# Performance work log

Measured on AMD Instinct MI355X. Metric: run time of the kernel, lower is better.

## Reference

```python
import jax, jax.numpy as jnp
import numpy as np
import math

D_MODEL = 1024
NUM_HEADS = 16
HEAD_DIM = D_MODEL // NUM_HEADS
BLOCK_SIZE = 64
THRESHOLD = 0.99


def setup_inputs() -> dict:
    key = jax.random.key(0)
    ks = jax.random.split(key, 12)
    B, S, D = 2, 2048, D_MODEL
    scale = 1.0 / math.sqrt(D)
    x = jax.random.normal(ks[0], (B, S, D), dtype=jnp.float32)
    G_ii = jax.random.uniform(ks[1], (B, S), dtype=jnp.float32)
    # Linear weights stored as [in, out]; applied as x @ W + b (matches nn.Linear math).
    Wq = jax.random.normal(ks[2], (D, D), dtype=jnp.float32) * scale
    bq = jnp.zeros((D,), dtype=jnp.float32)
    Wk = jax.random.normal(ks[3], (D, D), dtype=jnp.float32) * scale
    bk = jnp.zeros((D,), dtype=jnp.float32)
    Wv = jax.random.normal(ks[4], (D, D), dtype=jnp.float32) * scale
    bv = jnp.zeros((D,), dtype=jnp.float32)
    Wo = jax.random.normal(ks[5], (D, D), dtype=jnp.float32) * scale
    bo = jnp.zeros((D,), dtype=jnp.float32)
    return {"x": x, "G_ii": G_ii, "Wq": Wq, "bq": bq, "Wk": Wk, "bk": bk,
            "Wv": Wv, "bv": bv, "Wo": Wo, "bo": bo}


def reference(x, G_ii, Wq, bq, Wk, bk, Wv, bv, Wo, bo):
    B, S, D = x.shape
    H, hd, bs = NUM_HEADS, HEAD_DIM, BLOCK_SIZE
    nb = S // bs

    # Projections and head split: [B, H, S, hd]
    q = (x @ Wq + bq).reshape(B, S, H, hd).transpose(0, 2, 1, 3)
    k = (x @ Wk + bk).reshape(B, S, H, hd).transpose(0, 2, 1, 3)
    v = (x @ Wv + bv).reshape(B, S, H, hd).transpose(0, 2, 1, 3)

    # Per-query-block scattering energy keep mask: block kept iff max |G_ii| >= threshold
    energy = jnp.abs(G_ii)                              # [B, S]
    block_max = energy.reshape(B, nb, bs).max(axis=-1)  # [B, nb]
    keep = (block_max >= THRESHOLD)                     # [B, nb] bool
    row_keep = jnp.repeat(keep, bs, axis=1)             # [B, S]

    # Kept query blocks attend densely (non-causal) over all keys; skipped blocks output zero.
    scores = jnp.einsum('bhqd,bhkd->bhqk', q, k) / math.sqrt(hd)  # [B, H, S, S]
    attn = jax.nn.softmax(scores, axis=-1)
    out = jnp.einsum('bhqk,bhkd->bhqd', attn, v)                  # [B, H, S, hd]
    out = out * row_keep[:, None, :, None].astype(out.dtype)

    out = out.transpose(0, 2, 1, 3).reshape(B, S, D)
    return out @ Wo + bo
```

## Files before the change

### kernel.cpp

```cpp
#include <hip/hip_runtime.h>
#include <math.h>

#define D_MODEL   1024
#define NUM_HEADS 16
#define HEAD_DIM  64
#define BS        64
#define NB        32
#define S_LEN     2048
#define BATCH     2
#define M_ROWS    (BATCH * S_LEN)
#define THRESH    0.99f
#define SCEXP     0.18033688f
#define SPLITK    4
#define NSLOT     66
#define SLOTB     (NSLOT * 16)

typedef __attribute__((ext_vector_type(8))) short bf16x8;
typedef __attribute__((ext_vector_type(8))) _Float16 f16x8;
typedef __attribute__((ext_vector_type(2))) __fp16 fp16v2;
typedef __attribute__((ext_vector_type(4))) float f32x4;

__device__ __forceinline__ unsigned short f2bf(float f) {
    unsigned int u = __float_as_uint(f);
    u += 0x7fff + ((u >> 16) & 1);
    return (unsigned short)(u >> 16);
}

__device__ __forceinline__ unsigned int pkrtz(float a, float b) {
    fp16v2 r = __builtin_amdgcn_cvt_pkrtz(a, b);
    return __builtin_bit_cast(unsigned int, r);
}

__device__ __forceinline__ void gload16(const void* gptr, void* lptr) {
    __builtin_amdgcn_global_load_lds(
        (const __attribute__((address_space(1))) void*)gptr,
        (__attribute__((address_space(3))) void*)lptr, 16, 0, 0);
}

__global__ __launch_bounds__(256) void prep_kernel(
    const float* __restrict__ x, const float* __restrict__ G,
    const float* __restrict__ Wq, const float* __restrict__ Wk,
    const float* __restrict__ Wv, const float* __restrict__ Wo,
    unsigned short* __restrict__ xb, unsigned short* __restrict__ wcat,
    unsigned short* __restrict__ wot, int* __restrict__ keep, int* __restrict__ work)
{
    const int bid = blockIdx.x, tid = threadIdx.x;
    __shared__ float T[64][65];

    if (bid < 2048) {
        size_t i = ((size_t)bid * 256 + tid) * 8;
        float4 a = *(const float4*)(x + i);
        float4 b = *(const float4*)(x + i + 4);
        uint4 o;
        o.x = (unsigned int)f2bf(a.x) | ((unsigned int)f2bf(a.y) << 16);
        o.y = (unsigned int)f2bf(a.z) | ((unsigned int)f2bf(a.w) << 16);
        o.z = (unsigned int)f2bf(b.x) | ((unsigned int)f2bf(b.y) << 16);
        o.w = (unsigned int)f2bf(b.z) | ((unsigned int)f2bf(b.w) << 16);
        *(uint4*)(xb + i) = o;
    } else if (bid < 3072) {
        int i = bid - 2048;
        int mat = i >> 8, rem = i & 255;
        int k0 = (rem & 15) * 64, n0 = (rem >> 4) * 64;
        const float* W = (mat == 0) ? Wq : (mat == 1) ? Wk : (mat == 2) ? Wv : Wo;
        int rr = tid >> 4, c4 = (tid & 15) * 4;
        #pragma unroll
        for (int j = 0; j < 4; j++) {
            int row = rr + j * 16;
            float4 v = *(const float4*)(W + (size_t)(k0 + row) * 1024 + n0 + c4);
            T[row][c4 + 0] = v.x; T[row][c4 + 1] = v.y;
            T[row][c4 + 2] = v.z; T[row][c4 + 3] = v.w;
        }
        __syncthreads();
        unsigned short* dst = (mat < 3) ? (wcat + (size_t)mat * 1024 * 1024) : wot;
        #pragma unroll
        for (int j = 0; j < 4; j++) {
            int n = rr + j * 16;
            unsigned int lo = (unsigned int)f2bf(T[c4 + 0][n]) | ((unsigned int)f2bf(T[c4 + 1][n]) << 16);
            unsigned int hi = (unsigned int)f2bf(T[c4 + 2][n]) | ((unsigned int)f2bf(T[c4 + 3][n]) << 16);
            *(uint2*)(dst + (size_t)(n0 + n) * 1024 + k0 + c4) = make_uint2(lo, hi);
        }
    } else {
        if (tid < 64) {
            int t = tid;
            const float4* g = (const float4*)(G + (size_t)t * 64);
            float mx = 0.f;
            #pragma unroll
            for (int j = 0; j < 16; j++) {
                float4 v = g[j];
                mx = fmaxf(mx, fmaxf(fmaxf(fabsf(v.x), fabsf(v.y)), fmaxf(fabsf(v.z), fabsf(v.w))));
            }
            bool k = (mx >= THRESH);
            unsigned long long bal = __ballot(k);
            unsigned int mk0 = (unsigned int)bal, mk1 = (unsigned int)(bal >> 32);
            int nk0 = __popc(mk0), nk1 = __popc(mk1);
            int ND0 = (nk0 + 1) >> 1, ND1 = (nk1 + 1) >> 1;
            keep[t] = k ? 1 : 0;
            int tb = t & 31, bb = t >> 5;
            unsigned int mb = bb ? mk1 : mk0;
            unsigned int msk = (tb == 0) ? 0u : ((1u << tb) - 1u);
            int rank = __popc(mb & msk);
            int rd   = __popc(~mb & msk);
            int base = bb ? 2 * ND0 : 0;
            int dbase = 2 * ND0 + 2 * ND1;
            int doff = bb ? (32 - nk0) : 0;
            if (k)  work[1 + base + rank] = t;
            else    work[1 + dbase + doff + rd] = t | (1 << 8);
            if (t == 0) {
                work[0] = ND0 + ND1;
                if (nk0 & 1) work[1 + nk0] = (31 - __clz(mk0)) | (2 << 8);
                if (nk1 & 1) work[1 + 2 * ND0 + nk1] = (63 - __clz(mk1)) | (2 << 8);
                int total = dbase + (64 - nk0 - nk1);
                for (int j = total; j < NSLOT; j++) work[1 + j] = (2 << 8);
            }
        }
    }
}

__global__ __launch_bounds__(256, 3) void gemm_qkv(
    const unsigned short* __restrict__ A, const unsigned short* __restrict__ Bt,
    const float* __restrict__ bq, const float* __restrict__ bk, const float* __restrict__ bv,
    const int* __restrict__ keep, unsigned short* __restrict__ qk, unsigned short* __restrict__ vt)
{
    const int n0 = blockIdx.x * 128, m0 = blockIdx.y * 128;
    const int tid = threadIdx.x, w = tid >> 6, lane = tid & 63;
    const int quad = lane >> 4, l16 = lane & 15;
    const int wm = w >> 1, wn = w & 1;
    const int kindb = n0 >> 10;
    if (kindb == 0 && !(keep[2 * blockIdx.y] | keep[2 * blockIdx.y + 1])) return;

    __shared__ union {
        struct { unsigned short As[2][128 * 32]; unsigned short Bs[2][128 * 32]; } s;
        unsigned short qkr[128 * 136];
        unsigned short vr[128 * 136];
    } u;

    f32x4 acc[4][4];
    #pragma unroll
    for (int mt = 0; mt < 4; mt++)
        #pragma unroll
        for (int nt = 0; nt < 4; nt++) acc[mt][nt] = (f32x4){0.f, 0.f, 0.f, 0.f};

    #define QSTAGE(it_, p_)                                                             \
        {                                                                               \
            int k0_ = (it_) * 32;                                                       \
            _Pragma("unroll")                                                           \
            for (int j = 0; j < 2; j++) {                                               \
                int s_ = w * 128 + j * 64 + lane; int row = s_ >> 2, cl = s_ & 3;       \
                int c = cl ^ ((row >> 1) & 3);                                          \
                gload16(A + (size_t)(m0 + row) * 1024 + k0_ + c * 8,                    \
                        &u.s.As[p_][(w * 128 + j * 64) * 8]);                           \
            }                                                                           \
            _Pragma("unroll")                                                           \
            for (int j = 0; j < 2; j++) {                                               \
                int s_ = w * 128 + j * 64 + lane; int row = s_ >> 2, cl = s_ & 3;       \
                int c = cl ^ ((row >> 1) & 3);                                          \
                gload16(Bt + (size_t)(n0 + row) * 1024 + k0_ + c * 8,                   \
                        &u.s.Bs[p_][(w * 128 + j * 64) * 8]);                           \
            }                                                                           \
        }

    QSTAGE(0, 0)

    for (int it = 0; it < 32; it++) {
        const int p = it & 1;
        __syncthreads();
        if (it + 1 < 32) QSTAGE(it + 1, (it + 1) & 1)

        bf16x8 af[4], bfr[4];
        #pragma unroll
        for (int mt = 0; mt < 4; mt++) {
            int row = wm * 64 + mt * 16 + l16;
            int cl = quad ^ ((row >> 1) & 3);
            af[mt] = *(const bf16x8*)&u.s.As[p][(row * 4 + cl) * 8];
        }
        #pragma unroll
        for (int nt = 0; nt < 4; nt++) {
            int row = wn * 64 + nt * 16 + l16;
            int cl = quad ^ ((row >> 1) & 3);
            bfr[nt] = *(const bf16x8*)&u.s.Bs[p][(row * 4 + cl) * 8];
        }
        #pragma unroll
        for (int mt = 0; mt < 4; mt++)
            #pragma unroll
            for (int nt = 0; nt < 4; nt++)
                acc[mt][nt] = __builtin_amdgcn_mfma_f32_16x16x32_bf16(af[mt], bfr[nt], acc[mt][nt], 0, 0, 0);
    }
    __syncthreads();

    if (kindb < 2) {
        const float* bp = (kindb == 0) ? bq : bk;
        const float sc = (kindb == 0) ? SCEXP : 1.0f;
        #pragma unroll
        for (int nt = 0; nt < 4; nt++) {
            int coll = wn * 64 + nt * 16 + l16;
            float bb = bp[(n0 & 1023) + coll];
            #pragma unroll
            for (int mt = 0; mt < 4; mt++)
                #pragma unroll
                for (int r = 0; r < 4; r++) {
                    int row = wm * 64 + mt * 16 + quad * 4 + r;
                    u.qkr[row * 136 + coll] = f2bf((acc[mt][nt][r] + bb) * sc);
                }
        }
        __syncthreads();
        #pragma unroll
        for (int i = 0; i < 8; i++) {
            int s_ = tid + i * 256;
            int row = s_ >> 4, c16 = s_ & 15;
            uint4 v = *(const uint4*)&u.qkr[row * 136 + c16 * 8];
            *(uint4*)(qk + (size_t)(m0 + row) * 2048 + n0 + c16 * 8) = v;
        }
    } else {
        #pragma unroll
        for (int nt = 0; nt < 4; nt++) {
            int coll = wn * 64 + nt * 16 + l16;
            float bb = bv[(n0 - 2048) + coll];
            #pragma unroll
            for (int mt = 0; mt < 4; mt++) {
                int s0 = wm * 64 + mt * 16 + quad * 4;
                uint2 pv;
                pv.x = pkrtz(acc[mt][nt][0] + bb, acc[mt][nt][1] + bb);
                pv.y = pkrtz(acc[mt][nt][2] + bb, acc[mt][nt][3] + bb);
                *(uint2*)&u.vr[coll * 136 + s0] = pv;
            }
        }
        __syncthreads();
        const int b_ = m0 >> 11, sbase = m0 & 2047;
        #pragma unroll
        for (int i = 0; i < 8; i++) {
            int s_ = tid + i * 256;
            int coll = s_ >> 4, ch = s_ & 15;
            uint4 v = *(const uint4*)&u.vr[coll * 136 + ch * 8];
            int colg = n0 - 2048 + coll;
            int h_ = colg >> 6, d = colg & 63;
            *(uint4*)(vt + ((size_t)(b_ * NUM_HEADS + h_) * HEAD_DIM + d) * 2048 + sbase + ch * 8) = v;
        }
    }
}

__global__ __launch_bounds__(256, 4) void gemm_out(
    const unsigned short* __restrict__ A, const unsigned short* __restrict__ Bt,
    const float* __restrict__ bo, const int* __restrict__ keep, float* __restrict__ out)
{
    const int n0 = blockIdx.x * 64, m0 = blockIdx.y * 64;
    const int tid = threadIdx.x, w = tid >> 6, lane = tid & 63;
    const int quad = lane >> 4, l16 = lane & 15;
    const int wm = w >> 1, wn = w & 1;

    if (!keep[blockIdx.y]) {
        #pragma unroll
        for (int i = 0; i < 4; i++) {
            int s_ = tid + i * 256;
            int row = s_ >> 4, c = (s_ & 15) * 4;
            *(float4*)(out + (size_t)(m0 + row) * 1024 + n0 + c) = *(const float4*)(bo + n0 + c);
        }
        return;
    }

    __shared__ unsigned short Asl[2][64 * 32];
    __shared__ unsigned short Bsl[2][64 * 32];

    f32x4 acc[2][2];
    #pragma unroll
    for (int mt = 0; mt < 2; mt++)
        #pragma unroll
        for (int nt = 0; nt < 2; nt++) acc[mt][nt] = (f32x4){0.f, 0.f, 0.f, 0.f};

    #define OSTAGE(it_, p_)                                                             \
        {                                                                               \
            int k0_ = (it_) * 32;                                                       \
            int s_ = w * 64 + lane; int row = s_ >> 2, cl = s_ & 3;                     \
            int c = cl ^ ((row >> 1) & 3);                                              \
            gload16(A  + (size_t)(m0 + row) * 1024 + k0_ + c * 8, &Asl[p_][(w * 64) * 8]); \
            gload16(Bt + (size_t)(n0 + row) * 1024 + k0_ + c * 8, &Bsl[p_][(w * 64) * 8]); \
        }

    OSTAGE(0, 0)

    for (int it = 0; it < 32; it++) {
        const int p = it & 1;
        __syncthreads();
        if (it + 1 < 32) OSTAGE(it + 1, (it + 1) & 1)

        bf16x8 af[2], bfr[2];
        #pragma unroll
        for (int mt = 0; mt < 2; mt++) {
            int row = wm * 32 + mt * 16 + l16;
            int cl = quad ^ ((row >> 1) & 3);
            af[mt] = *(const bf16x8*)&Asl[p][(row * 4 + cl) * 8];
        }
        #pragma unroll
        for (int nt = 0; nt < 2; nt++) {
            int row = wn * 32 + nt * 16 + l16;
            int cl = quad ^ ((row >> 1) & 3);
            bfr[nt] = *(const bf16x8*)&Bsl[p][(row * 4 + cl) * 8];
        }
        #pragma unroll
        for (int mt = 0; mt < 2; mt++)
            #pragma unroll
            for (int nt = 0; nt < 2; nt++)
                acc[mt][nt] = __builtin_amdgcn_mfma_f32_16x16x32_bf16(af[mt], bfr[nt], acc[mt][nt], 0, 0, 0);
    }

    #pragma unroll
    for (int nt = 0; nt < 2; nt++) {
        int col = n0 + wn * 32 + nt * 16 + l16;
        float bb = bo[col];
        #pragma unroll
        for (int mt = 0; mt < 2; mt++) {
            int mb = m0 + wm * 32 + mt * 16 + quad * 4;
            #pragma unroll
            for (int r = 0; r < 4; r++)
                out[(size_t)(mb + r) * 1024 + col] = acc[mt][nt][r] + bb;
        }
    }
}

__global__ __launch_bounds__(256, 3) void attn_kernel(
    const unsigned short* __restrict__ qk, const unsigned short* __restrict__ Vtg,
    const int* __restrict__ work,
    unsigned short* __restrict__ opart, float* __restrict__ lpart)
{
    const int bx = blockIdx.x, half = blockIdx.y;
    const int dpair = bx >> 4, h = bx & 15;
    const int tid  = threadIdx.x;
    const int w    = tid >> 6, lane = tid & 63;
    const int quad = lane >> 4, l16 = lane & 15;

    if (dpair >= work[0]) return;
    const int j0 = 2 * dpair, j1 = j0 + 1;
    const int t0 = work[1 + j0] & 63, t1 = work[1 + j1] & 63;
    const int b = t0 >> 5, qb0 = t0 & 31, qb1 = t1 & 31;

    __shared__ unsigned short Kbuf[2][BS * HEAD_DIM];
    __shared__ unsigned short Vbuf[2][HEAD_DIM * BS];
    __shared__ unsigned short Pt[4][2][16 * 64];

    const int KEYS = S_LEN / SPLITK;
    const int NCH  = KEYS / BS;
    const unsigned short* Qb = qk + (size_t)(b * S_LEN) * 2048 + h * 64;
    const unsigned short* Kb = qk + (size_t)(b * S_LEN + half * KEYS) * 2048 + 1024 + h * 64;
    const unsigned short* Vb = Vtg + (size_t)(b * NUM_HEADS + h) * HEAD_DIM * 2048 + half * KEYS;

    const int qrow0 = qb0 * BS + w * 16 + l16;
    const int qrow1 = qb1 * BS + w * 16 + l16;
    bf16x8 qf0[2], qf1[2];
    #pragma unroll
    for (int ks = 0; ks < 2; ks++) {
        qf0[ks] = *(const bf16x8*)(Qb + (size_t)qrow0 * 2048 + ks * 32 + quad * 8);
        qf1[ks] = *(const bf16x8*)(Qb + (size_t)qrow1 * 2048 + ks * 32 + quad * 8);
    }

    f32x4 o0[4], o1[4];
    #pragma unroll
    for (int mt = 0; mt < 4; mt++) { o0[mt] = (f32x4){0.f,0.f,0.f,0.f}; o1[mt] = (f32x4){0.f,0.f,0.f,0.f}; }
    float l0 = 0.f, l1 = 0.f;

    const int sA = w * 128 + lane, sB = sA + 64;
    const int rA = sA >> 3, cA = (sA & 7) ^ (rA & 7);
    const int rB = sB >> 3, cB = (sB & 7) ^ (rB & 7);
    const size_t koA = (size_t)rA * 2048 + cA * 8, koB = (size_t)rB * 2048 + cB * 8;

    uint4 kr0, kr1, vr0, vr1;
    #define LOADREGS(kc_)                                                       \
        {                                                                       \
            const unsigned short* kg_ = Kb + (size_t)(kc_) * BS * 2048;         \
            const unsigned short* vg_ = Vb + (size_t)(kc_) * BS;                \
            kr0 = *(const uint4*)(kg_ + koA); kr1 = *(const uint4*)(kg_ + koB); \
            vr0 = *(const uint4*)(vg_ + koA); vr1 = *(const uint4*)(vg_ + koB); \
        }
    #define WRITELDS(pb_)                                                       \
        {                                                                       \
            *(uint4*)&Kbuf[pb_][(size_t)sA * 8] = kr0;                          \
            *(uint4*)&Kbuf[pb_][(size_t)sB * 8] = kr1;                          \
            *(uint4*)&Vbuf[pb_][(size_t)sA * 8] = vr0;                          \
            *(uint4*)&Vbuf[pb_][(size_t)sB * 8] = vr1;                          \
        }

    LOADREGS(0)
    WRITELDS(0)
    __syncthreads();

    #pragma unroll
    for (int kc = 0; kc < NCH; kc++) {
        const int p = kc & 1;
        if (kc + 1 < NCH) LOADREGS(kc + 1)

        f32x4 st0[4], st1[4];
        __builtin_amdgcn_s_setprio(1);
        #pragma unroll
        for (int mt = 0; mt < 4; mt++) {
            f32x4 a0 = {0.f,0.f,0.f,0.f}, a1 = {0.f,0.f,0.f,0.f};
            #pragma unroll
            for (int ks = 0; ks < 2; ks++) {
                int kk = mt * 16 + l16;
                bf16x8 kf = *(const bf16x8*)&Kbuf[p][(size_t)(kk * 8 + ((ks * 4 + quad) ^ (kk & 7))) * 8];
                a0 = __builtin_amdgcn_mfma_f32_16x16x32_bf16(kf, qf0[ks], a0, 0, 0, 0);
                a1 = __builtin_amdgcn_mfma_f32_16x16x32_bf16(kf, qf1[ks], a1, 0, 0, 0);
            }
            st0[mt] = a0; st1[mt] = a1;
        }
        __builtin_amdgcn_s_setprio(0);

        float sum0 = 0.f, sum1 = 0.f;
        #pragma unroll
        for (int mt = 0; mt < 4; mt++) {
            int c16 = 2 * mt + (quad >> 1);
            int off = (c16 ^ (l16 & 7)) * 8 + (quad & 1) * 4;
            float e00 = __builtin_amdgcn_exp2f(st0[mt][0]);
            float e01 = __builtin_amdgcn_exp2f(st0[mt][1]);
            float e02 = __builtin_amdgcn_exp2f(st0[mt][2]);
            float e03 = __builtin_amdgcn_exp2f(st0[mt][3]);
            sum0 += (e00 + e01) + (e02 + e03);
            *(uint2*)&Pt[w][0][l16 * 64 + off] = make_uint2(pkrtz(e00, e01), pkrtz(e02, e03));
            float e10 = __builtin_amdgcn_exp2f(st1[mt][0]);
            float e11 = __builtin_amdgcn_exp2f(st1[mt][1]);
            float e12 = __builtin_amdgcn_exp2f(st1[mt][2]);
            float e13 = __builtin_amdgcn_exp2f(st1[mt][3]);
            sum1 += (e10 + e11) + (e12 + e13);
            *(uint2*)&Pt[w][1][l16 * 64 + off] = make_uint2(pkrtz(e10, e11), pkrtz(e12, e13));
        }
        sum0 += __shfl_xor(sum0, 16, 64);
        sum0 += __shfl_xor(sum0, 32, 64);
        sum1 += __shfl_xor(sum1, 16, 64);
        sum1 += __shfl_xor(sum1, 32, 64);
        l0 += sum0; l1 += sum1;

        __builtin_amdgcn_s_setprio(1);
        #pragma unroll
        for (int ks = 0; ks < 2; ks++) {
            int poff = ((4 * ks + quad) ^ (l16 & 7)) * 8;
            f16x8 pf0 = *(const f16x8*)&Pt[w][0][l16 * 64 + poff];
            f16x8 pf1 = *(const f16x8*)&Pt[w][1][l16 * 64 + poff];
            #pragma unroll
            for (int mt = 0; mt < 4; mt++) {
                int d = mt * 16 + l16;
                f16x8 vf = *(const f16x8*)&Vbuf[p][(size_t)(d * 8 + ((ks * 4 + quad) ^ (d & 7))) * 8];
                o0[mt] = __builtin_amdgcn_mfma_f32_16x16x32_f16(vf, pf0, o0[mt], 0, 0, 0);
                o1[mt] = __builtin_amdgcn_mfma_f32_16x16x32_f16(vf, pf1, o1[mt], 0, 0, 0);
            }
        }
        __builtin_amdgcn_s_setprio(0);

        if (kc + 1 < NCH) {
            WRITELDS(p ^ 1)
            __syncthreads();
        }
    }

    {
        unsigned short* ob = opart + ((size_t)(half * SLOTB + j0 * 16 + h)) * 4096 + tid * 16;
        uint4 w0, w1;
        w0.x = pkrtz(o0[0][0], o0[0][1]); w0.y = pkrtz(o0[0][2], o0[0][3]);
        w0.z = pkrtz(o0[1][0], o0[1][1]); w0.w = pkrtz(o0[1][2], o0[1][3]);
        w1.x = pkrtz(o0[2][0], o0[2][1]); w1.y = pkrtz(o0[2][2], o0[2][3]);
        w1.z = pkrtz(o0[3][0], o0[3][1]); w1.w = pkrtz(o0[3][2], o0[3][3]);
        *(uint4*)ob = w0;
        *(uint4*)(ob + 8) = w1;
    }
    {
        unsigned short* ob = opart + ((size_t)(half * SLOTB + j1 * 16 + h)) * 4096 + tid * 16;
        uint4 w0, w1;
        w0.x = pkrtz(o1[0][0], o1[0][1]); w0.y = pkrtz(o1[0][2], o1[0][3]);
        w0.z = pkrtz(o1[1][0], o1[1][1]); w0.w = pkrtz(o1[1][2], o1[1][3]);
        w1.x = pkrtz(o1[2][0], o1[2][1]); w1.y = pkrtz(o1[2][2], o1[2][3]);
        w1.z = pkrtz(o1[3][0], o1[3][1]); w1.w = pkrtz(o1[3][2], o1[3][3]);
        *(uint4*)ob = w0;
        *(uint4*)(ob + 8) = w1;
    }
    if (quad == 0) {
        lpart[((size_t)half * SLOTB + j0 * 16 + h) * 64 + w * 16 + l16] = l0;
        lpart[((size_t)half * SLOTB + j1 * 16 + h) * 64 + w * 16 + l16] = l1;
    }
}

__global__ __launch_bounds__(256) void attn_combine(
    const unsigned short* __restrict__ opart, const float* __restrict__ lpart,
    const int* __restrict__ work, unsigned short* __restrict__ attn_out)
{
    const int bx = blockIdx.x;
    const int pair = bx >> 4, h = bx & 15;
    const int tid  = threadIdx.x;
    const int w    = tid >> 6, lane = tid & 63;
    const int quad = lane >> 4, l16 = lane & 15;

    const int e = work[1 + pair];
    const int flag = e >> 8, t = e & 63;
    if (flag == 2) return;
    const int b = t >> 5, qblk = t & 31;
    unsigned short* ablk = attn_out + ((size_t)(b * S_LEN + qblk * BS)) * D_MODEL + h * HEAD_DIM;

    if (flag == 1) {
        uint4 z = make_uint4(0, 0, 0, 0);
        #pragma unroll
        for (int i = 0; i < 2; i++) {
            int u = tid + i * 256;
            int row = u >> 3, c8 = (u & 7) * 8;
            *(uint4*)(ablk + (size_t)row * D_MODEL + c8) = z;
        }
        return;
    }

    __shared__ float Obuf[4][HEAD_DIM * 17];

    float osum[16];
    #pragma unroll
    for (int j = 0; j < 16; j++) osum[j] = 0.f;
    float lsum = 0.f;
    #pragma unroll
    for (int hf = 0; hf < SPLITK; hf++) {
        const f16x8* pp = (const f16x8*)(opart + ((size_t)hf * SLOTB + bx) * 4096 + tid * 16);
        f16x8 a0 = pp[0], a1 = pp[1];
        #pragma unroll
        for (int j = 0; j < 8; j++) {
            osum[j]     += (float)a0[j];
            osum[8 + j] += (float)a1[j];
        }
        lsum += lpart[((size_t)hf * SLOTB + bx) * 64 + w * 16 + l16];
    }
    float inv = 1.0f / lsum;

    #pragma unroll
    for (int mt = 0; mt < 4; mt++)
        #pragma unroll
        for (int r = 0; r < 4; r++)
            Obuf[w][(mt * 16 + quad * 4 + r) * 17 + l16] = osum[mt * 4 + r] * inv;
    #pragma unroll
    for (int i = 0; i < 4; i++) {
        int uu = lane + 64 * i;
        int row = uu >> 4, d4 = (uu & 15) * 4;
        float x0 = Obuf[w][(d4 + 0) * 17 + row];
        float x1 = Obuf[w][(d4 + 1) * 17 + row];
        float x2 = Obuf[w][(d4 + 2) * 17 + row];
        float x3 = Obuf[w][(d4 + 3) * 17 + row];
        unsigned int lo = (unsigned int)f2bf(x0) | ((unsigned int)f2bf(x1) << 16);
        unsigned int hi = (unsigned int)f2bf(x2) | ((unsigned int)f2bf(x3) << 16);
        *(uint2*)(ablk + (size_t)(w * 16 + row) * D_MODEL + d4) = make_uint2(lo, hi);
    }
}

extern "C" void kernel_launch(void* const* d_in, const int* in_sizes, int n_in,
                              void* d_out, int out_size, void* d_ws, size_t ws_size,
                              hipStream_t stream) {
    const float* x  = (const float*)d_in[0];
    const float* G  = (const float*)d_in[1];
    const float* Wq = (const float*)d_in[2];
    const float* bq = (const float*)d_in[3];
    const float* Wk = (const float*)d_in[4];
    const float* bk = (const float*)d_in[5];
    const float* Wv = (const float*)d_in[6];
    const float* bv = (const float*)d_in[7];
    const float* Wo = (const float*)d_in[8];
    const float* bo = (const float*)d_in[9];
    float* out = (float*)d_out;

    char* wsp = (char*)d_ws;
    int* keep = (int*)wsp;
    int* work = keep + 64;
    unsigned short* xb    = (unsigned short*)(wsp + 1024);
    unsigned short* wcat  = xb + (size_t)M_ROWS * D_MODEL;
    unsigned short* wot   = wcat + (size_t)3 * 1024 * 1024;
    unsigned short* qk    = wot + (size_t)1024 * 1024;
    unsigned short* vt    = qk + (size_t)M_ROWS * 2048;
    unsigned short* attnb = vt + (size_t)BATCH * NUM_HEADS * HEAD_DIM * 2048;
    unsigned short* opart = attnb + (size_t)M_ROWS * D_MODEL;
    float* lpart = (float*)(opart + (size_t)SPLITK * SLOTB * 4096);

    prep_kernel<<<3073, 256, 0, stream>>>(x, G, Wq, Wk, Wv, Wo, xb, wcat, wot, keep, work);

    gemm_qkv<<<dim3(3072 / 128, M_ROWS / 128), 256, 0, stream>>>(
        xb, wcat, bq, bk, bv, keep, qk, vt);

    attn_kernel<<<dim3(32 * 16, SPLITK), 256, 0, stream>>>(qk, vt, work, opart, lpart);
    attn_combine<<<SLOTB, 256, 0, stream>>>(opart, lpart, work, attnb);

    gemm_out<<<dim3(1024 / 64, M_ROWS / 64), 256, 0, stream>>>(attnb, wot, bo, keep, out);
}
```

Measured before the change: 178.4 us.

## Read K/V fragments directly from global memory instead of staging in LDS

Removes the double-buffered LDS staging of K and V tiles and the per-chunk __syncthreads. Each wave now loads its MFMA K and V fragments straight from global memory, relying on the caches for reuse across the four waves. With less shared memory the launch bound is raised to 4 blocks per SM. The risk is four times the global/L2 traffic per block and exposed load latency, since nothing is prefetched ahead of the MFMAs.

After: 242.0 us. 35.6% more time.

```diff
diff --git a/kernel.cpp b/kernel.cpp
--- a/kernel.cpp
+++ b/kernel.cpp
@@ -316,7 +316,7 @@
     }
 }
 
-__global__ __launch_bounds__(256, 3) void attn_kernel(
+__global__ __launch_bounds__(256, 4) void attn_kernel(
     const unsigned short* __restrict__ qk, const unsigned short* __restrict__ Vtg,
     const int* __restrict__ work,
     unsigned short* __restrict__ opart, float* __restrict__ lpart)
@@ -332,8 +332,6 @@
     const int t0 = work[1 + j0] & 63, t1 = work[1 + j1] & 63;
     const int b = t0 >> 5, qb0 = t0 & 31, qb1 = t1 & 31;
 
-    __shared__ unsigned short Kbuf[2][BS * HEAD_DIM];
-    __shared__ unsigned short Vbuf[2][HEAD_DIM * BS];
     __shared__ unsigned short Pt[4][2][16 * 64];
 
     const int KEYS = S_LEN / SPLITK;
@@ -356,36 +354,8 @@
     for (int mt = 0; mt < 4; mt++) { o0[mt] = (f32x4){0.f,0.f,0.f,0.f}; o1[mt] = (f32x4){0.f,0.f,0.f,0.f}; }
     float l0 = 0.f, l1 = 0.f;
 
-    const int sA = w * 128 + lane, sB = sA + 64;
-    const int rA = sA >> 3, cA = (sA & 7) ^ (rA & 7);
-    const int rB = sB >> 3, cB = (sB & 7) ^ (rB & 7);
-    const size_t koA = (size_t)rA * 2048 + cA * 8, koB = (size_t)rB * 2048 + cB * 8;
-
-    uint4 kr0, kr1, vr0, vr1;
-    #define LOADREGS(kc_)                                                       \
-        {                                                                       \
-            const unsigned short* kg_ = Kb + (size_t)(kc_) * BS * 2048;         \
-            const unsigned short* vg_ = Vb + (size_t)(kc_) * BS;                \
-            kr0 = *(const uint4*)(kg_ + koA); kr1 = *(const uint4*)(kg_ + koB); \
-            vr0 = *(const uint4*)(vg_ + koA); vr1 = *(const uint4*)(vg_ + koB); \
-        }
-    #define WRITELDS(pb_)                                                       \
-        {                                                                       \
-            *(uint4*)&Kbuf[pb_][(size_t)sA * 8] = kr0;                          \
-            *(uint4*)&Kbuf[pb_][(size_t)sB * 8] = kr1;                          \
-            *(uint4*)&Vbuf[pb_][(size_t)sA * 8] = vr0;                          \
-            *(uint4*)&Vbuf[pb_][(size_t)sB * 8] = vr1;                          \
-        }
-
-    LOADREGS(0)
-    WRITELDS(0)
-    __syncthreads();
-
     #pragma unroll
     for (int kc = 0; kc < NCH; kc++) {
-        const int p = kc & 1;
-        if (kc + 1 < NCH) LOADREGS(kc + 1)
-
         f32x4 st0[4], st1[4];
         __builtin_amdgcn_s_setprio(1);
         #pragma unroll
@@ -393,8 +363,8 @@
             f32x4 a0 = {0.f,0.f,0.f,0.f}, a1 = {0.f,0.f,0.f,0.f};
             #pragma unroll
             for (int ks = 0; ks < 2; ks++) {
-                int kk = mt * 16 + l16;
-                bf16x8 kf = *(const bf16x8*)&Kbuf[p][(size_t)(kk * 8 + ((ks * 4 + quad) ^ (kk & 7))) * 8];
+                int kk = kc * BS + mt * 16 + l16;
+                bf16x8 kf = *(const bf16x8*)(Kb + (size_t)kk * 2048 + ks * 32 + quad * 8);
                 a0 = __builtin_amdgcn_mfma_f32_16x16x32_bf16(kf, qf0[ks], a0, 0, 0, 0);
                 a1 = __builtin_amdgcn_mfma_f32_16x16x32_bf16(kf, qf1[ks], a1, 0, 0, 0);
             }
@@ -435,17 +405,12 @@
             #pragma unroll
             for (int mt = 0; mt < 4; mt++) {
                 int d = mt * 16 + l16;
-                f16x8 vf = *(const f16x8*)&Vbuf[p][(size_t)(d * 8 + ((ks * 4 + quad) ^ (d & 7))) * 8];
+                f16x8 vf = *(const f16x8*)(Vb + (size_t)d * 2048 + kc * BS + ks * 32 + quad * 8);
                 o0[mt] = __builtin_amdgcn_mfma_f32_16x16x32_f16(vf, pf0, o0[mt], 0, 0, 0);
                 o1[mt] = __builtin_amdgcn_mfma_f32_16x16x32_f16(vf, pf1, o1[mt], 0, 0, 0);
             }
         }
         __builtin_amdgcn_s_setprio(0);
-
-        if (kc + 1 < NCH) {
-            WRITELDS(p ^ 1)
-            __syncthreads();
-        }
     }
 
     {
```
